# Kernel optimization log

Hardware: AMD Instinct MI355X
Metric: run time of the kernel (lower is better)

The kernel has to match this reference:

```python
import jax, jax.numpy as jnp
import numpy as np

B, S, H, NH = 2, 2048, 1024, 16
HD = H // NH  # 64


def setup_inputs() -> dict:
    key = jax.random.key(0)
    ks = jax.random.split(key, 9)
    w = lambda k: jax.random.normal(k, (H, H), dtype=jnp.float32) * 0.02  # torch Linear weight [out,in]
    b = lambda k: jax.random.normal(k, (H,), dtype=jnp.float32) * 0.02
    return {
        "hidden_states": jax.random.normal(ks[0], (B, S, H), dtype=jnp.float32),
        "Wq": w(ks[1]), "bq": b(ks[2]),
        "Wk": w(ks[3]), "bk": b(ks[4]),
        "Wv": w(ks[5]), "bv": b(ks[6]),
        "Wo": w(ks[7]), "bo": b(ks[8]),
    }


def reference(hidden_states, Wq, bq, Wk, bk, Wv, bv, Wo, bo):
    b, s, h = hidden_states.shape
    nh, hd = NH, h // NH

    def proj(W, bias):
        y = hidden_states @ W.T + bias  # torch Linear: x W^T + b
        return y.reshape(b, s, nh, hd).transpose(0, 2, 1, 3)  # [b, h, s, d]

    q = proj(Wq, bq)
    k = proj(Wk, bk)
    v = proj(Wv, bv)

    scale = jnp.sqrt(jnp.asarray(hd, dtype=q.dtype))
    scores = jnp.einsum("bhqd,bhkd->bhqk", q, k) / scale  # [b, h, s, s]
    pos = jnp.arange(s)
    causal = pos[:, None] < pos[None, :]  # True where masked (key after query)
    scores = jnp.where(causal[None, None], -jnp.inf, scores)
    attn = jax.nn.softmax(scores, axis=-1)
    out = jnp.einsum("bhqk,bhkd->bhqd", attn, v)
    out = out.transpose(0, 2, 1, 3).reshape(b, s, h)
    return out @ Wo.T + bo
```

## Files before the change

### kernel.cpp

```cpp
#include <hip/hip_runtime.h>
#include <stdint.h>

typedef __bf16 bf16;
typedef __attribute__((ext_vector_type(2))) __bf16 bf16x2;
typedef __attribute__((ext_vector_type(4))) __bf16 bf16x4;
typedef __attribute__((ext_vector_type(8))) __bf16 bf16x8;
typedef __attribute__((ext_vector_type(4))) float f32x4;
typedef __attribute__((ext_vector_type(4))) short s16x4;

#define B_  2
#define S_  2048
#define H_  1024
#define NH_ 16
#define HD_ 64
#define STV 136

__device__ __forceinline__ void glds16(const bf16* g, bf16* l) {
  __builtin_amdgcn_global_load_lds(
      (const __attribute__((address_space(1))) uint32_t*)g,
      (__attribute__((address_space(3))) uint32_t*)l, 16, 0, 0);
}

__device__ __forceinline__ f32x4 pv_mfma(bf16x4 a, bf16x4 b, f32x4 c) {
#if __has_builtin(__builtin_amdgcn_mfma_f32_16x16x16bf16_1k)
  union U { bf16x4 h; s16x4 s; };
  U ua; ua.h = a;
  U ub; ub.h = b;
  return __builtin_amdgcn_mfma_f32_16x16x16bf16_1k(ua.s, ub.s, c, 0, 0, 0);
#else
  f32x4 d;
  asm volatile("v_mfma_f32_16x16x16_bf16 %0, %1, %2, %3\n\ts_nop 7\n\ts_nop 7"
               : "=v"(d) : "v"(a), "v"(b), "v"(c));
  return d;
#endif
}

__global__ __launch_bounds__(256) void cvt_f32_bf16(
    const float* __restrict__ s0, bf16* __restrict__ d0, int n0,
    const float* __restrict__ s1, bf16* __restrict__ d1,
    const float* __restrict__ s2, bf16* __restrict__ d2,
    const float* __restrict__ s3, bf16* __restrict__ d3,
    const float* __restrict__ s4, bf16* __restrict__ d4, int nw)
{
  const float* s; bf16* d; int n;
  switch (blockIdx.y) {
    case 0:  s = s0; d = d0; n = n0; break;
    case 1:  s = s1; d = d1; n = nw; break;
    case 2:  s = s2; d = d2; n = nw; break;
    case 3:  s = s3; d = d3; n = nw; break;
    default: s = s4; d = d4; n = nw; break;
  }
  const int i = (blockIdx.x * 256 + threadIdx.x) * 8;
  if (i >= n) return;
  float4 v0 = *(const float4*)(s + i);
  float4 v1 = *(const float4*)(s + i + 4);
  bf16x8 o;
  o[0] = (bf16)v0.x; o[1] = (bf16)v0.y; o[2] = (bf16)v0.z; o[3] = (bf16)v0.w;
  o[4] = (bf16)v1.x; o[5] = (bf16)v1.y; o[6] = (bf16)v1.z; o[7] = (bf16)v1.w;
  *(bf16x8*)(d + i) = o;
}

template <typename TY>
__global__ __launch_bounds__(256) void gemm_bt_bias(
    const bf16* __restrict__ X,
    const bf16* __restrict__ W0, const bf16* __restrict__ W1, const bf16* __restrict__ W2,
    const float* __restrict__ b0, const float* __restrict__ b1, const float* __restrict__ b2,
    TY* __restrict__ Y0, TY* __restrict__ Y1, TY* __restrict__ Y2,
    int M, int N, int K)
{
  const bf16* W; const float* bias; TY* Y;
  if (blockIdx.z == 0)      { W = W0; bias = b0; Y = Y0; }
  else if (blockIdx.z == 1) { W = W1; bias = b1; Y = Y1; }
  else                      { W = W2; bias = b2; Y = Y2; }

  __shared__ __align__(16) bf16 As[2][128 * 32];
  __shared__ __align__(16) bf16 Bs[2][128 * 32];

  const int tid  = threadIdx.x;
  const int lane = tid & 63;
  const int wave = tid >> 6;
  const int m0 = blockIdx.y * 128;
  const int n0 = blockIdx.x * 128;
  const int wm = (wave >> 1) * 64;
  const int wn = (wave & 1) * 64;

  const int r0 = tid >> 2,            c0 = (tid & 3) * 8;
  const int r1 = (256 + tid) >> 2,    c1 = ((256 + tid) & 3) * 8;
  const int cb0 = (wave * 64) * 8;
  const int cb1 = (256 + wave * 64) * 8;

  f32x4 acc[4][4] = {};

  glds16(X + (size_t)(m0 + r0) * K + c0, &As[0][cb0]);
  glds16(W + (size_t)(n0 + r0) * K + c0, &Bs[0][cb0]);
  glds16(X + (size_t)(m0 + r1) * K + c1, &As[0][cb1]);
  glds16(W + (size_t)(n0 + r1) * K + c1, &Bs[0][cb1]);

  int pb = 0;
  for (int k0 = 0; k0 < K; k0 += 32, pb ^= 1) {
    __syncthreads();

    if (k0 + 32 < K) {
      const int kn = k0 + 32;
      glds16(X + (size_t)(m0 + r0) * K + kn + c0, &As[pb ^ 1][cb0]);
      glds16(W + (size_t)(n0 + r0) * K + kn + c0, &Bs[pb ^ 1][cb0]);
      glds16(X + (size_t)(m0 + r1) * K + kn + c1, &As[pb ^ 1][cb1]);
      glds16(W + (size_t)(n0 + r1) * K + kn + c1, &Bs[pb ^ 1][cb1]);
    }

    bf16x8 a[4], b[4];
#pragma unroll
    for (int i = 0; i < 4; ++i)
      a[i] = *(const bf16x8*)&As[pb][(wm + i * 16 + (lane & 15)) * 32 + (lane >> 4) * 8];
#pragma unroll
    for (int i = 0; i < 4; ++i)
      b[i] = *(const bf16x8*)&Bs[pb][(wn + i * 16 + (lane & 15)) * 32 + (lane >> 4) * 8];
#pragma unroll
    for (int mi = 0; mi < 4; ++mi)
#pragma unroll
      for (int ni = 0; ni < 4; ++ni)
        acc[mi][ni] = __builtin_amdgcn_mfma_f32_16x16x32_bf16(a[mi], b[ni], acc[mi][ni], 0, 0, 0);
  }

#pragma unroll
  for (int mi = 0; mi < 4; ++mi) {
    const int row = m0 + wm + mi * 16 + (lane >> 4) * 4;
#pragma unroll
    for (int ni = 0; ni < 4; ++ni) {
      const int col = n0 + wn + ni * 16 + (lane & 15);
      const float bv = bias[col];
#pragma unroll
      for (int r = 0; r < 4; ++r)
        Y[(size_t)(row + r) * N + col] = (TY)(acc[mi][ni][r] + bv);
    }
  }
}


__device__ __forceinline__ void attn_tile_step(
    const bf16* Ksb, const bf16* Vtb, const bf16x8 bq[2], int qrow, int k0,
    bool maskit, float& mr, float& lr, f32x4 oacc[4], int l15, int quad)
{
  const float SCL = 0.125f * 1.44269504f;

  f32x4 sacc[8] = {};
  __builtin_amdgcn_s_setprio(1);
#pragma unroll
  for (int ks = 0; ks < 2; ++ks) {
#pragma unroll
    for (int mb = 0; mb < 8; ++mb) {
      const int row = mb * 16 + l15;
      const int ch  = (ks * 4 + quad) ^ (l15 & 7);
      bf16x8 ak = *(const bf16x8*)&Ksb[row * 64 + ch * 8];
      sacc[mb] = __builtin_amdgcn_mfma_f32_16x16x32_bf16(ak, bq[ks], sacc[mb], 0, 0, 0);
    }
  }
  __builtin_amdgcn_s_setprio(0);

  if (maskit) {
#pragma unroll
    for (int mb = 0; mb < 8; ++mb) {
      const int kb = k0 + mb * 16 + quad * 4;
#pragma unroll
      for (int r = 0; r < 4; ++r) {
        const float s = sacc[mb][r] * SCL;
        sacc[mb][r] = (kb + r > qrow) ? -1e30f : s;
      }
    }
  } else {
#pragma unroll
    for (int mb = 0; mb < 8; ++mb)
#pragma unroll
      for (int r = 0; r < 4; ++r)
        sacc[mb][r] = sacc[mb][r] * SCL;
  }

  float mx = -1e30f;
#pragma unroll
  for (int mb = 0; mb < 8; ++mb)
    mx = fmaxf(mx, fmaxf(fmaxf(sacc[mb][0], sacc[mb][1]),
                         fmaxf(sacc[mb][2], sacc[mb][3])));
  mx = fmaxf(mx, __shfl_xor(mx, 16, 64));
  mx = fmaxf(mx, __shfl_xor(mx, 32, 64));
  const float mnew  = fmaxf(mr, mx);
  const float alpha = __builtin_amdgcn_exp2f(mr - mnew);
  mr = mnew;

  float sum = 0.0f;
  bf16x4 pwv[8];
#pragma unroll
  for (int mb = 0; mb < 8; ++mb) {
#pragma unroll
    for (int r = 0; r < 4; ++r) {
      const float p = __builtin_amdgcn_exp2f(sacc[mb][r] - mnew);
      sum += p;
      pwv[mb][r] = (bf16)p;
    }
  }
  sum += __shfl_xor(sum, 16, 64);
  sum += __shfl_xor(sum, 32, 64);
  lr = lr * alpha + sum;
#pragma unroll
  for (int db = 0; db < 4; ++db)
#pragma unroll
    for (int r = 0; r < 4; ++r) oacc[db][r] *= alpha;

  __builtin_amdgcn_s_setprio(1);
#pragma unroll
  for (int mb = 0; mb < 8; ++mb) {
#pragma unroll
    for (int db = 0; db < 4; ++db) {
      bf16x4 av = *(const bf16x4*)&Vtb[(db * 16 + l15) * STV + mb * 16 + quad * 4];
      oacc[db] = pv_mfma(av, pwv[mb], oacc[db]);
    }
  }
  __builtin_amdgcn_s_setprio(0);
}

__global__ __launch_bounds__(256, 2) void attn_causal(
    const bf16* __restrict__ Q, const bf16* __restrict__ K,
    const bf16* __restrict__ V, bf16* __restrict__ O)
{
  const int lin  = blockIdx.x;
  const int slot = lin >> 3;
  const int bh   = (lin & 7) * 4 + (slot >> 4);
  const int pair = slot & 15;
  const int b    = bh >> 4;
  const int h    = bh & 15;

  const int tid  = threadIdx.x;
  const int lane = tid & 63;
  const int wave = tid >> 6;
  const int quad = lane >> 4;
  const int l15  = lane & 15;
  const size_t headoff = (size_t)b * S_ * H_ + (size_t)h * HD_;
  const bf16* Kp = K + headoff;
  const bf16* Vp = V + headoff;

  __shared__ __align__(16) bf16 Ks[2][128 * 64];
  __shared__ __align__(16) bf16 Vt[2][64 * STV];

  const int qlo = pair, qhi = 31 - pair;
  const int nl  = (qlo >> 1) + 1;
  const int nh  = (qhi >> 1) + 1;
  const int qrowL = qlo * 64 + wave * 16 + l15;
  const int qrowH = qhi * 64 + wave * 16 + l15;

  bf16x8 bqL[2], bqH[2];
  bqL[0] = *(const bf16x8*)(Q + headoff + (size_t)qrowL * H_ + quad * 8);
  bqL[1] = *(const bf16x8*)(Q + headoff + (size_t)qrowL * H_ + 32 + quad * 8);
  bqH[0] = *(const bf16x8*)(Q + headoff + (size_t)qrowH * H_ + quad * 8);
  bqH[1] = *(const bf16x8*)(Q + headoff + (size_t)qrowH * H_ + 32 + quad * 8);

  const int vr = lane * 2;
  const int vc = wave * 16;

#define STAGE_K(k0_, buf_)                                                  \
  {                                                                         \
    _Pragma("unroll")                                                       \
    for (int i = 0; i < 4; ++i) {                                           \
      const int n = i * 256 + tid;                                          \
      const int row = n >> 3;                                               \
      const int cg  = (n & 7) ^ (row & 7);                                  \
      glds16(Kp + (size_t)((k0_) + row) * H_ + cg * 8,                      \
             &Ks[buf_][(i * 256 + wave * 64) * 8]);                         \
    }                                                                       \
  }

#define LOAD_V(k0_)                                                         \
  {                                                                         \
    vreg[0] = *(const bf16x8*)(Vp + (size_t)((k0_) + vr) * H_ + vc);        \
    vreg[1] = *(const bf16x8*)(Vp + (size_t)((k0_) + vr) * H_ + vc + 8);    \
    vreg[2] = *(const bf16x8*)(Vp + (size_t)((k0_) + vr + 1) * H_ + vc);    \
    vreg[3] = *(const bf16x8*)(Vp + (size_t)((k0_) + vr + 1) * H_ + vc + 8);\
  }

#define WRITE_V(buf_)                                                       \
  {                                                                         \
    _Pragma("unroll")                                                       \
    for (int e = 0; e < 8; ++e) {                                           \
      bf16x2 p0; p0[0] = vreg[0][e]; p0[1] = vreg[2][e];                    \
      *(bf16x2*)&Vt[buf_][(vc + e) * STV + vr] = p0;                        \
      bf16x2 p1; p1[0] = vreg[1][e]; p1[1] = vreg[3][e];                    \
      *(bf16x2*)&Vt[buf_][(vc + 8 + e) * STV + vr] = p1;                    \
    }                                                                       \
  }

  bf16x8 vreg[4];

  STAGE_K(0, 0);
  LOAD_V(0);
  WRITE_V(0);
  __syncthreads();

  float mrL = -1e30f, lrL = 0.0f, mrH = -1e30f, lrH = 0.0f;
  f32x4 oL[4] = {}, oH[4] = {};

  for (int it = 0; it < nh; ++it) {
    const int c = it & 1;
    const bool pre = (it + 1 < nh);

    if (pre) {
      STAGE_K((it + 1) * 128, c ^ 1);
      LOAD_V((it + 1) * 128);
    }

    attn_tile_step(Ks[c], Vt[c], bqH, qrowH, it * 128, it == nh - 1,
                   mrH, lrH, oH, l15, quad);
    if (it < nl)
      attn_tile_step(Ks[c], Vt[c], bqL, qrowL, it * 128, it == nl - 1,
                     mrL, lrL, oL, l15, quad);

    if (pre) {
      WRITE_V(c ^ 1);
      __syncthreads();
    }
  }

  const float invL = 1.0f / lrL;
#pragma unroll
  for (int db = 0; db < 4; ++db) {
    bf16x4 o;
#pragma unroll
    for (int r = 0; r < 4; ++r) o[r] = (bf16)(oL[db][r] * invL);
    *(bf16x4*)(O + headoff + (size_t)qrowL * H_ + db * 16 + quad * 4) = o;
  }
  const float invH = 1.0f / lrH;
#pragma unroll
  for (int db = 0; db < 4; ++db) {
    bf16x4 o;
#pragma unroll
    for (int r = 0; r < 4; ++r) o[r] = (bf16)(oH[db][r] * invH);
    *(bf16x4*)(O + headoff + (size_t)qrowH * H_ + db * 16 + quad * 4) = o;
  }
#undef STAGE_K
#undef LOAD_V
#undef WRITE_V
}

extern "C" void kernel_launch(void* const* d_in, const int* in_sizes, int n_in,
                              void* d_out, int out_size, void* d_ws, size_t ws_size,
                              hipStream_t stream) {
  const float* hs = (const float*)d_in[0];
  const float* Wq = (const float*)d_in[1]; const float* bq = (const float*)d_in[2];
  const float* Wk = (const float*)d_in[3]; const float* bk = (const float*)d_in[4];
  const float* Wv = (const float*)d_in[5]; const float* bv = (const float*)d_in[6];
  const float* Wo = (const float*)d_in[7]; const float* bo = (const float*)d_in[8];
  float* out = (float*)d_out;

  const size_t elems = (size_t)B_ * S_ * H_;
  const size_t wel   = (size_t)H_ * H_;
  bf16* hsb = (bf16*)d_ws;
  bf16* AO  = hsb;
  bf16* Wqb = hsb + elems;
  bf16* Wkb = Wqb + wel;
  bf16* Wvb = Wkb + wel;
  bf16* Wob = Wvb + wel;
  bf16* Qw  = Wob + wel;
  bf16* Kw  = Qw + elems;
  bf16* Vw  = Kw + elems;

  cvt_f32_bf16<<<dim3(2048, 5), dim3(256), 0, stream>>>(
      hs, hsb, (int)elems, Wq, Wqb, Wk, Wkb, Wv, Wvb, Wo, Wob, (int)wel);

  const int M = B_ * S_;
  gemm_bt_bias<bf16><<<dim3(H_ / 128, M / 128, 3), dim3(256), 0, stream>>>(
      hsb, Wqb, Wkb, Wvb, bq, bk, bv, Qw, Kw, Vw, M, H_, H_);

  attn_causal<<<dim3(512), dim3(256), 0, stream>>>(Qw, Kw, Vw, AO);

  gemm_bt_bias<float><<<dim3(H_ / 128, M / 128, 1), dim3(256), 0, stream>>>(
      AO, Wob, Wob, Wob, bo, bo, bo, out, out, out, M, H_, H_);
}
```

Measured before the change: 199.3 us.

## Fold softmax scale into Q projection, lazy rescale, swizzle V transpose layout

Moves the 1/sqrt(d)*log2e scale into the Q projection epilogue so the attention kernel skips a per-score multiply. Adds lazy online-softmax rescaling: the running max is updated, and the output rescaled, only when some lane's new max exceeds the old one by more than 8 (log2 units). Replaces the padded V-transpose LDS stride with an XOR-swizzled 128-wide layout to avoid bank conflicts without padding. Risks: Q is rounded to bf16 after scaling, and starting the running max at 0 lets exp2 values grow up to 256x before rescaling, which could affect precision.

After: 201.1 us. No clear change (+0.9%).

```diff
diff --git a/kernel.cpp b/kernel.cpp
--- a/kernel.cpp
+++ b/kernel.cpp
@@ -13,7 +13,6 @@
 #define H_  1024
 #define NH_ 16
 #define HD_ 64
-#define STV 136
 
 __device__ __forceinline__ void glds16(const bf16* g, bf16* l) {
   __builtin_amdgcn_global_load_lds(
@@ -66,12 +65,13 @@
     const bf16* __restrict__ W0, const bf16* __restrict__ W1, const bf16* __restrict__ W2,
     const float* __restrict__ b0, const float* __restrict__ b1, const float* __restrict__ b2,
     TY* __restrict__ Y0, TY* __restrict__ Y1, TY* __restrict__ Y2,
+    float ys0, float ys1, float ys2,
     int M, int N, int K)
 {
-  const bf16* W; const float* bias; TY* Y;
-  if (blockIdx.z == 0)      { W = W0; bias = b0; Y = Y0; }
-  else if (blockIdx.z == 1) { W = W1; bias = b1; Y = Y1; }
-  else                      { W = W2; bias = b2; Y = Y2; }
+  const bf16* W; const float* bias; TY* Y; float ysc;
+  if (blockIdx.z == 0)      { W = W0; bias = b0; Y = Y0; ysc = ys0; }
+  else if (blockIdx.z == 1) { W = W1; bias = b1; Y = Y1; ysc = ys1; }
+  else                      { W = W2; bias = b2; Y = Y2; ysc = ys2; }
 
   __shared__ __align__(16) bf16 As[2][128 * 32];
   __shared__ __align__(16) bf16 Bs[2][128 * 32];
@@ -131,7 +131,7 @@
       const float bv = bias[col];
 #pragma unroll
       for (int r = 0; r < 4; ++r)
-        Y[(size_t)(row + r) * N + col] = (TY)(acc[mi][ni][r] + bv);
+        Y[(size_t)(row + r) * N + col] = (TY)((acc[mi][ni][r] + bv) * ysc);
     }
   }
 }
@@ -141,8 +141,6 @@
     const bf16* Ksb, const bf16* Vtb, const bf16x8 bq[2], int qrow, int k0,
     bool maskit, float& mr, float& lr, f32x4 oacc[4], int l15, int quad)
 {
-  const float SCL = 0.125f * 1.44269504f;
-
   f32x4 sacc[8] = {};
   __builtin_amdgcn_s_setprio(1);
 #pragma unroll
@@ -162,17 +160,9 @@
     for (int mb = 0; mb < 8; ++mb) {
       const int kb = k0 + mb * 16 + quad * 4;
 #pragma unroll
-      for (int r = 0; r < 4; ++r) {
-        const float s = sacc[mb][r] * SCL;
-        sacc[mb][r] = (kb + r > qrow) ? -1e30f : s;
-      }
-    }
-  } else {
-#pragma unroll
-    for (int mb = 0; mb < 8; ++mb)
-#pragma unroll
       for (int r = 0; r < 4; ++r)
-        sacc[mb][r] = sacc[mb][r] * SCL;
+        if (kb + r > qrow) sacc[mb][r] = -1e30f;
+    }
   }
 
   float mx = -1e30f;
@@ -182,39 +172,46 @@
                          fmaxf(sacc[mb][2], sacc[mb][3])));
   mx = fmaxf(mx, __shfl_xor(mx, 16, 64));
   mx = fmaxf(mx, __shfl_xor(mx, 32, 64));
-  const float mnew  = fmaxf(mr, mx);
-  const float alpha = __builtin_amdgcn_exp2f(mr - mnew);
-  mr = mnew;
 
   float sum = 0.0f;
   bf16x4 pwv[8];
 #pragma unroll
   for (int mb = 0; mb < 8; ++mb) {
+    bf16x4 pw;
 #pragma unroll
     for (int r = 0; r < 4; ++r) {
-      const float p = __builtin_amdgcn_exp2f(sacc[mb][r] - mnew);
+      const float p = __builtin_amdgcn_exp2f(sacc[mb][r] - mr);
       sum += p;
-      pwv[mb][r] = (bf16)p;
-    }
+      pw[r] = (bf16)p;
+    }
+    pwv[mb] = pw;
   }
   sum += __shfl_xor(sum, 16, 64);
   sum += __shfl_xor(sum, 32, 64);
-  lr = lr * alpha + sum;
-#pragma unroll
-  for (int db = 0; db < 4; ++db)
-#pragma unroll
-    for (int r = 0; r < 4; ++r) oacc[db][r] *= alpha;
 
   __builtin_amdgcn_s_setprio(1);
 #pragma unroll
   for (int mb = 0; mb < 8; ++mb) {
 #pragma unroll
     for (int db = 0; db < 4; ++db) {
-      bf16x4 av = *(const bf16x4*)&Vtb[(db * 16 + l15) * STV + mb * 16 + quad * 4];
+      const int vch = ((mb * 4 + quad) ^ (l15 & 7)) * 4;
+      bf16x4 av = *(const bf16x4*)&Vtb[(db * 16 + l15) * 128 + vch];
       oacc[db] = pv_mfma(av, pwv[mb], oacc[db]);
     }
   }
   __builtin_amdgcn_s_setprio(0);
+
+  lr += sum;
+  if (!__all(mx <= mr + 8.0f)) {
+    const float mnew  = fmaxf(mr, mx);
+    const float alpha = __builtin_amdgcn_exp2f(mr - mnew);
+    lr *= alpha;
+#pragma unroll
+    for (int db = 0; db < 4; ++db)
+#pragma unroll
+      for (int r = 0; r < 4; ++r) oacc[db][r] *= alpha;
+    mr = mnew;
+  }
 }
 
 __global__ __launch_bounds__(256, 2) void attn_causal(
@@ -238,7 +235,7 @@
   const bf16* Vp = V + headoff;
 
   __shared__ __align__(16) bf16 Ks[2][128 * 64];
-  __shared__ __align__(16) bf16 Vt[2][64 * STV];
+  __shared__ __align__(16) bf16 Vt[2][64 * 128];
 
   const int qlo = pair, qhi = 31 - pair;
   const int nl  = (qlo >> 1) + 1;
@@ -279,10 +276,11 @@
   {                                                                         \
     _Pragma("unroll")                                                       \
     for (int e = 0; e < 8; ++e) {                                           \
+      const int sw = (((vr >> 2) ^ e) * 4) + (vr & 3);                      \
       bf16x2 p0; p0[0] = vreg[0][e]; p0[1] = vreg[2][e];                    \
-      *(bf16x2*)&Vt[buf_][(vc + e) * STV + vr] = p0;                        \
+      *(bf16x2*)&Vt[buf_][(vc + e) * 128 + sw] = p0;                        \
       bf16x2 p1; p1[0] = vreg[1][e]; p1[1] = vreg[3][e];                    \
-      *(bf16x2*)&Vt[buf_][(vc + 8 + e) * STV + vr] = p1;                    \
+      *(bf16x2*)&Vt[buf_][(vc + 8 + e) * 128 + sw] = p1;                    \
     }                                                                       \
   }
 
@@ -293,7 +291,7 @@
   WRITE_V(0);
   __syncthreads();
 
-  float mrL = -1e30f, lrL = 0.0f, mrH = -1e30f, lrH = 0.0f;
+  float mrL = 0.0f, lrL = 0.0f, mrH = 0.0f, lrH = 0.0f;
   f32x4 oL[4] = {}, oH[4] = {};
 
   for (int it = 0; it < nh; ++it) {
@@ -364,11 +362,12 @@
       hs, hsb, (int)elems, Wq, Wqb, Wk, Wkb, Wv, Wvb, Wo, Wob, (int)wel);
 
   const int M = B_ * S_;
+  const float QSCL = 0.125f * 1.44269504f;
   gemm_bt_bias<bf16><<<dim3(H_ / 128, M / 128, 3), dim3(256), 0, stream>>>(
-      hsb, Wqb, Wkb, Wvb, bq, bk, bv, Qw, Kw, Vw, M, H_, H_);
+      hsb, Wqb, Wkb, Wvb, bq, bk, bv, Qw, Kw, Vw, QSCL, 1.0f, 1.0f, M, H_, H_);
 
   attn_causal<<<dim3(512), dim3(256), 0, stream>>>(Qw, Kw, Vw, AO);
 
   gemm_bt_bias<float><<<dim3(H_ / 128, M / 128, 1), dim3(256), 0, stream>>>(
-      AO, Wob, Wob, Wob, bo, bo, bo, out, out, out, M, H_, H_);
-}
+      AO, Wob, Wob, Wob, bo, bo, bo, out, out, out, 1.0f, 1.0f, 1.0f, M, H_, H_);
+}
```
